# Optimization experiments

Measured on AMD Instinct MI355X. Metric: run time of the kernel, lower is better.

## Reference

```python
import jax, jax.numpy as jnp
import numpy as np

N, D, O, H, T, S, R, BN = 4096, 256, 256, 256, 512, 8, 4, 2  # nodes, in, out, hidden, text_len, adj_size, relations used, basis_num


def setup_inputs() -> dict:
    key = jax.random.key(0)
    ks = jax.random.split(key, 16)
    sc = 0.05
    return {
        "entity_embeddings": jax.random.normal(ks[0], (N, D), jnp.float32) * sc,
        "text_encodings": jax.random.normal(ks[1], (1, T, 2 * H), jnp.float32) * sc,
        "adj_to_use": jnp.arange(R, dtype=jnp.int32),
        "adj_masks": jax.random.randint(ks[2], (R, N, N), 0, 2, dtype=jnp.int32),
        "text_guids": jax.random.normal(ks[3], (S, 2 * H), jnp.float32) * sc,
        "graph_guids_1": jax.random.normal(ks[4], (S, D), jnp.float32) * sc,
        "graph_guids_2": jax.random.normal(ks[5], (S, D), jnp.float32) * sc,
        "guid_a": jax.random.normal(ks[6], (S,), jnp.float32),
        "basis_V": jax.random.normal(ks[7], (D, BN, O), jnp.float32) * sc,
        "basis_b": jax.random.normal(ks[8], (S, BN), jnp.float32) * sc,
        "W_1": jax.random.normal(ks[9], (2 * H, D), jnp.float32) * sc,
        "W_2": jax.random.normal(ks[10], (2 * H, D), jnp.float32) * sc,
        "ln_gamma": jnp.ones((O,), jnp.float32),
        "ln_beta": jnp.zeros((O,), jnp.float32),
    }


def reference(entity_embeddings, text_encodings, adj_to_use, adj_masks,
              text_guids, graph_guids_1, graph_guids_2, guid_a,
              basis_V, basis_b, W_1, W_2, ln_gamma, ln_beta):
    te = text_encodings[0]                                  # [T, 2H] (batch of 1)
    tg = text_guids[adj_to_use]                             # [R, 2H]
    # text attention: softmax over T, per relation
    att = jax.nn.softmax(te @ tg.T, axis=0)                 # [T, R]
    context = att.T @ te                                    # [R, 2H]
    c1 = context @ W_1                                      # [R, D]
    c2 = context @ W_2
    ga = jax.nn.sigmoid(guid_a[adj_to_use])[:, None]        # [R, 1]
    g1 = ga * graph_guids_1[adj_to_use] + (1.0 - ga) * c1   # [R, D]
    g2 = ga * graph_guids_2[adj_to_use] + (1.0 - ga) * c2
    s1 = entity_embeddings @ g1.T                           # [N, R]
    s2 = entity_embeddings @ g2.T
    # A[r,i,j] = s1[i,r] + s2[j,r], masked softmax over j
    A = s1.T[:, :, None] + s2.T[:, None, :]                 # [R, N, N]
    A = jnp.where(adj_masks == 1, A, jnp.float32(-1e10))
    A = jax.nn.softmax(A, axis=-1)
    fused = jnp.einsum('rij,jd->rid', A, entity_embeddings) # [R, N, D]
    # torch.cat over relations on last dim -> column index r*D + d
    fused_cat = jnp.transpose(fused, (1, 0, 2)).reshape(N, R * D)
    # torch.matmul([R,BN],[D,BN,O]) -> [D,R,O], then .view(R*D, O) (row index d*R + r)
    bb = basis_b[adj_to_use]                                # [R, BN]
    W = jnp.einsum('rb,dbo->dro', bb, basis_V).reshape(D * R, O)
    out = fused_cat @ W                                     # [N, O]
    mu = jnp.mean(out, axis=-1, keepdims=True)
    var = jnp.var(out, axis=-1, keepdims=True)
    out = (out - mu) / jnp.sqrt(var + 1e-5) * ln_gamma + ln_beta
    return jax.nn.relu(out)
```

## Files before the change

kernel.cpp:

```cpp
#include <hip/hip_runtime.h>
#include <hip/hip_bf16.h>


typedef unsigned short u16;
typedef short bf16x8 __attribute__((ext_vector_type(8)));
typedef float f32x4 __attribute__((ext_vector_type(4)));
typedef float f32x8 __attribute__((ext_vector_type(8)));
typedef int   v4i   __attribute__((ext_vector_type(4)));
typedef unsigned int v2u __attribute__((ext_vector_type(2)));

#define G2_OFF    0
#define SC_OFF    4096
#define CTX_OFF   16384
#define WRT_OFF   69632
#define FPT_OFF   593920
#define FUSED_OFF 9506816
#define CAN_OFF   26284032

__device__ __forceinline__ float b2f(u16 u) {
    union { unsigned int i; float f; } v; v.i = ((unsigned int)u) << 16; return v.f;
}
__device__ __forceinline__ u16 f2b(float f) {
    union { float f; unsigned int i; } v; v.f = f;
    return (u16)((v.i + 0x7FFFu + ((v.i >> 16) & 1u)) >> 16);
}
__device__ __forceinline__ float rawf(const void* p, bool isbf, int i) {
    return isbf ? b2f(((const u16*)p)[i]) : ((const float*)p)[i];
}
__device__ __forceinline__ f32x8 raw8(const void* p, bool isbf, int i8) {
    f32x8 o;
    if (isbf) {
        bf16x8 v = *(const bf16x8*)((const u16*)p + i8);
        #pragma unroll
        for (int k = 0; k < 8; ++k) o[k] = b2f((u16)v[k]);
    } else {
        const float* f = (const float*)p + i8;
        float4 a = *(const float4*)f, b = *(const float4*)(f + 4);
        o[0] = a.x; o[1] = a.y; o[2] = a.z; o[3] = a.w;
        o[4] = b.x; o[5] = b.y; o[6] = b.z; o[7] = b.w;
    }
    return o;
}

__global__ __launch_bounds__(512) void k_front(
    const void* __restrict__ ent_raw, const void* __restrict__ te_raw,
    const int* __restrict__ adj, const void* __restrict__ tg_raw,
    const void* __restrict__ bV_raw, const void* __restrict__ bb_raw,
    const unsigned* __restrict__ graw,
    u16* __restrict__ ent_can, float* __restrict__ sc_ws, u16* __restrict__ wrt)
{
    bool isbf = (graw[0] == 0x3F803F80u);
    int b = blockIdx.x, tid = threadIdx.x;
    if (b < 256) {
        int base = b * 4096 + tid;
        if (isbf) {
            const u16* s = (const u16*)ent_raw;
            #pragma unroll
            for (int k = 0; k < 8; ++k) { int i = base + k * 512; ent_can[i] = s[i]; }
        } else {
            const float* s = (const float*)ent_raw;
            #pragma unroll
            for (int k = 0; k < 8; ++k) { int i = base + k * 512; ent_can[i] = f2b(s[i]); }
        }
        return;
    }
    if (b < 384) {
        int b2 = b - 256;
        int r = b2 >> 5, cq = b2 & 31;
        int c = cq * 8 + (tid >> 6);
        int dq = tid & 63;
        int a[4] = {adj[0], adj[1], adj[2], adj[3]};
        #pragma unroll
        for (int dd = 0; dd < 4; ++dd) {
            float w = 0.f;
            #pragma unroll
            for (int bi = 0; bi < 2; ++bi)
                w += rawf(bb_raw, isbf, a[dd] * 2 + bi) *
                     rawf(bV_raw, isbf, ((64 * r + dq) * 2 + bi) * 256 + c);
            wrt[(r * 256 + c) * 256 + dq * 4 + dd] = f2b(w);
        }
        return;
    }
    __shared__ float s_tg[4 * 512];
    int a[4] = {adj[0], adj[1], adj[2], adj[3]};
    for (int idx = tid; idx < 2048; idx += 512) {
        int r = idx >> 9, h = idx & 511;
        s_tg[r * 512 + h] = rawf(tg_raw, isbf, a[r] * 512 + h);
    }
    __syncthreads();
    int b2 = b - 384;
    int t = b2 * 16 + (tid >> 5);
    int h0 = (tid & 31) * 16;
    float s[4] = {0.f, 0.f, 0.f, 0.f};
    #pragma unroll
    for (int half = 0; half < 2; ++half) {
        f32x8 v = raw8(te_raw, isbf, t * 512 + h0 + half * 8);
        #pragma unroll
        for (int k = 0; k < 8; ++k) {
            float tv = v[k]; int h = h0 + half * 8 + k;
            #pragma unroll
            for (int r = 0; r < 4; ++r) s[r] += tv * s_tg[r * 512 + h];
        }
    }
    #pragma unroll
    for (int r = 0; r < 4; ++r) {
        #pragma unroll
        for (int m = 16; m > 0; m >>= 1) s[r] += __shfl_xor(s[r], m);
    }
    if ((tid & 31) == 0) {
        #pragma unroll
        for (int r = 0; r < 4; ++r) sc_ws[t * 4 + r] = s[r];
    }
}

__global__ __launch_bounds__(256) void k_ctx(const void* __restrict__ te_raw,
                                             const float* __restrict__ sc_ws,
                                             const unsigned* __restrict__ graw,
                                             float* __restrict__ ctx_ws) {
    bool isbf = (graw[0] == 0x3F803F80u);
    __shared__ float s_att[512];
    __shared__ float s_red[256];
    __shared__ float s_part[32 * 8];
    int b = blockIdx.x, tid = threadIdx.x;
    int r = b >> 6, hc = b & 63;
    float v0 = sc_ws[tid * 4 + r], v1 = sc_ws[(tid + 256) * 4 + r];
    s_red[tid] = fmaxf(v0, v1);
    __syncthreads();
    for (int st = 128; st > 0; st >>= 1) {
        if (tid < st) s_red[tid] = fmaxf(s_red[tid], s_red[tid + st]);
        __syncthreads();
    }
    float mx = s_red[0];
    __syncthreads();
    float e0 = __expf(v0 - mx), e1 = __expf(v1 - mx);
    s_red[tid] = e0 + e1;
    __syncthreads();
    for (int st = 128; st > 0; st >>= 1) {
        if (tid < st) s_red[tid] += s_red[tid + st];
        __syncthreads();
    }
    float rdn = 1.f / s_red[0];
    __syncthreads();
    s_att[tid] = e0 * rdn;
    s_att[tid + 256] = e1 * rdn;
    __syncthreads();
    int hl = tid & 7, tq = tid >> 3;
    int h = hc * 8 + hl;
    float acc = 0.f;
    #pragma unroll 4
    for (int t = tq * 16; t < tq * 16 + 16; ++t)
        acc += s_att[t] * rawf(te_raw, isbf, t * 512 + h);
    s_part[tq * 8 + hl] = acc;
    __syncthreads();
    if (tid < 8) {
        float c = 0.f;
        #pragma unroll
        for (int s = 0; s < 32; ++s) c += s_part[s * 8 + tid];
        ctx_ws[r * 512 + hc * 8 + tid] = c;
    }
}

__global__ __launch_bounds__(256) void k_g2(const float* __restrict__ ctx_ws,
                                            const int* __restrict__ adj,
                                            const void* __restrict__ W2_raw,
                                            const void* __restrict__ gg2_raw,
                                            const void* __restrict__ ga_raw,
                                            const unsigned* __restrict__ graw,
                                            float* __restrict__ g2ws) {
    bool isbf = (graw[0] == 0x3F803F80u);
    __shared__ float s_ctx[512];
    __shared__ float s_p[2][128];
    int b = blockIdx.x, tid = threadIdx.x;
    int r = b >> 1, dh = b & 1;
    for (int idx = tid; idx < 512; idx += 256) s_ctx[idx] = ctx_ws[r * 512 + idx];
    __syncthreads();
    int dl = tid & 127, th = tid >> 7;
    int d = dh * 128 + dl;
    float acc = 0.f;
    for (int h = th * 256; h < th * 256 + 256; ++h)
        acc += s_ctx[h] * rawf(W2_raw, isbf, h * 256 + d);
    s_p[th][dl] = acc;
    __syncthreads();
    if (th == 0) {
        float tot = s_p[0][dl] + s_p[1][dl];
        int ar = adj[r];
        float gav = 1.f / (1.f + expf(-rawf(ga_raw, isbf, ar)));
        g2ws[r * 256 + d] = gav * rawf(gg2_raw, isbf, ar * 256 + d) + (1.f - gav) * tot;
    }
}

__global__ __launch_bounds__(512) void k_fplus(const u16* __restrict__ entity,
                                               const u16* __restrict__ wrt,
                                               const float* __restrict__ g2ws,
                                               u16* __restrict__ fpt) {
    int b = blockIdx.x, tid = threadIdx.x;
    int r = b & 3, ct = (b >> 2) & 3, jt = b >> 4;
    int c0 = ct * 64, j0 = jt * 256;
    __shared__ __align__(16) u16 lw[64 * 264];
    __shared__ float sg2[256];
    __shared__ float sE[256];
    const u16* wr = wrt + (r * 256 + c0) * 256;
    #pragma unroll
    for (int k = 0; k < 4; ++k) {
        int ci = tid + k * 512; int row = ci >> 5, off = (ci & 31) * 8;
        *(v4i*)(&lw[row * 264 + off]) = *(const v4i*)(wr + row * 256 + off);
    }
    if (tid < 256) sg2[tid] = g2ws[r * 256 + tid];
    __syncthreads();
    int wv = tid >> 6, lane = tid & 63, ln = lane & 15, q = lane >> 4;
    {
        float gl0 = sg2[lane * 4 + 0], gl1 = sg2[lane * 4 + 1];
        float gl2 = sg2[lane * 4 + 2], gl3 = sg2[lane * 4 + 3];
        #pragma unroll 4
        for (int i = 0; i < 32; ++i) {
            int row = j0 + wv * 32 + i;
            v2u e4 = *(const v2u*)(entity + row * 256 + lane * 4);
            float s = b2f((u16)(e4.x & 0xFFFFu)) * gl0
                    + b2f((u16)(e4.x >> 16))     * gl1
                    + b2f((u16)(e4.y & 0xFFFFu)) * gl2
                    + b2f((u16)(e4.y >> 16))     * gl3;
            #pragma unroll
            for (int m = 32; m > 0; m >>= 1) s += __shfl_xor(s, m);
            if (lane == 0) sE[wv * 32 + i] = expf(s);
        }
    }
    __syncthreads();
    f32x4 acc[4][2] = {};
    for (int ks = 0; ks < 8; ++ks) {
        bf16x8 afr[4], bfr[2];
        #pragma unroll
        for (int mt = 0; mt < 4; ++mt)
            afr[mt] = *(const bf16x8*)(&lw[(mt * 16 + ln) * 264 + ks * 32 + q * 8]);
        #pragma unroll
        for (int nt = 0; nt < 2; ++nt) {
            int j = j0 + (wv * 2 + nt) * 16 + ln;
            bfr[nt] = *(const bf16x8*)(entity + j * 256 + ks * 32 + q * 8);
        }
        #pragma unroll
        for (int mt = 0; mt < 4; ++mt)
            #pragma unroll
            for (int nt = 0; nt < 2; ++nt)
                acc[mt][nt] = __builtin_amdgcn_mfma_f32_16x16x32_bf16(afr[mt], bfr[nt], acc[mt][nt], 0, 0, 0);
    }
    #pragma unroll
    for (int nt = 0; nt < 2; ++nt) {
        int jl = (wv * 2 + nt) * 16 + ln;
        int j = j0 + jl;
        float e2j = sE[jl];
        int kt = j >> 5, kk = j & 31;
        u16* dst = fpt + (((size_t)(r * 128 + kt)) * 272 << 5);
        #pragma unroll
        for (int mt = 0; mt < 4; ++mt)
            #pragma unroll
            for (int reg = 0; reg < 4; ++reg) {
                int c = c0 + mt * 16 + q * 4 + reg;
                dst[(c << 5) + kk] = f2b(acc[mt][nt][reg] * e2j);
            }
    }
    if (ct == 0) {
        #pragma unroll
        for (int s = 0; s < 8; ++s) {
            int l = s * 512 + tid;
            int kk = l & 31, cl = (l >> 5) & 15, ktl = l >> 9;
            int kt = jt * 8 + ktl;
            fpt[(((size_t)(r * 128 + kt) * 272 + 256 + cl) << 5) + kk] =
                (cl == 0) ? f2b(sE[ktl * 32 + kk]) : (u16)0;
        }
    }
}

__global__ __launch_bounds__(512) void k_big(const int* __restrict__ masks,
                                             const u16* __restrict__ fpt,
                                             float* __restrict__ fused) {
    __shared__ __align__(16) u16 lm[2][64 * 32];
    __shared__ __align__(16) u16 lf[2][272 * 32];
    __shared__ float lden[64];
    int b = blockIdx.x, tid = threadIdx.x;
    int xcd = b & 7; int r = xcd & 3;
    int it = (b >> 3) + ((xcd >> 2) << 5);
    long i0 = (long)it * 64;
    const int* mbase = masks + ((long)r << 24) + i0 * 4096;
    const u16* fbase = fpt + (size_t)r * 128 * 272 * 32;
    int wave = tid >> 6, lane = tid & 63, ln = lane & 15, q = lane >> 4;
    int mg = wave >> 2, ng = wave & 3;
    int swb = (ln >> 1) & 3;
    int rq = (q ^ swb) * 8;
    int srow = tid >> 2, sch = tid & 3;
    int ssw = (sch ^ ((srow >> 1) & 3)) * 8;

    f32x4 acc[2][4] = {};
    f32x4 accD0 = {}, accD1 = {};

    struct Slot { v4i pm0, pm1, f0, f1, f2; };
    Slot s0, s1, s2, s3;
    auto load_slot = [&](int kt, Slot& s) {
        const u16* su = fbase + (size_t)kt * 8704;
        s.f0 = *(const v4i*)(su + tid * 8);
        s.f1 = *(const v4i*)(su + (tid + 512) * 8);
        if (tid < 64) s.f2 = *(const v4i*)(su + (tid + 1024) * 8);
        if (tid < 256) {
            const int* mp = mbase + srow * 4096 + kt * 32 + sch * 8;
            s.pm0 = __builtin_nontemporal_load((const v4i*)mp);
            s.pm1 = __builtin_nontemporal_load((const v4i*)(mp + 4));
        }
    };
    auto stage = [&](int par, const Slot& s) {
        u16* dst = &lf[par][0];
        *(v4i*)(dst + srow * 32 + ssw) = s.f0;
        *(v4i*)(dst + (128 + srow) * 32 + ssw) = s.f1;
        if (tid < 64) *(v4i*)(dst + (256 + srow) * 32 + ssw) = s.f2;
        if (tid < 256) {
            unsigned m0 = (unsigned)s.pm0.x * 0x3F80u, m1 = (unsigned)s.pm0.y * 0x3F80u;
            unsigned m2 = (unsigned)s.pm0.z * 0x3F80u, m3 = (unsigned)s.pm0.w * 0x3F80u;
            unsigned m4 = (unsigned)s.pm1.x * 0x3F80u, m5 = (unsigned)s.pm1.y * 0x3F80u;
            unsigned m6 = (unsigned)s.pm1.z * 0x3F80u, m7 = (unsigned)s.pm1.w * 0x3F80u;
            v4i w;
            w.x = (int)(m0 | (m1 << 16)); w.y = (int)(m2 | (m3 << 16));
            w.z = (int)(m4 | (m5 << 16)); w.w = (int)(m6 | (m7 << 16));
            *(v4i*)(&lm[par][srow * 32 + ssw]) = w;
        }
    };
    auto step = [&](int k, Slot& sM, Slot& sF) {
        const u16* msrc = &lm[k & 1][0];
        const u16* src  = &lf[k & 1][0];
        bf16x8 a0 = *(const bf16x8*)(msrc + (mg * 32 + ln) * 32 + rq);
        bf16x8 a1 = *(const bf16x8*)(msrc + (mg * 32 + 16 + ln) * 32 + rq);
        if (k + 1 < 128) stage((k + 1) & 1, sF);
        if (k + 4 < 128) load_slot(k + 4, sM);
        #pragma unroll
        for (int nt = 0; nt < 4; ++nt) {
            bf16x8 bf = *(const bf16x8*)(src + ((ng * 4 + nt) * 16 + ln) * 32 + rq);
            acc[0][nt] = __builtin_amdgcn_mfma_f32_16x16x32_bf16(a0, bf, acc[0][nt], 0, 0, 0);
            acc[1][nt] = __builtin_amdgcn_mfma_f32_16x16x32_bf16(a1, bf, acc[1][nt], 0, 0, 0);
        }
        if (ng == 3) {
            bf16x8 bf = *(const bf16x8*)(src + (256 + ln) * 32 + rq);
            accD0 = __builtin_amdgcn_mfma_f32_16x16x32_bf16(a0, bf, accD0, 0, 0, 0);
            accD1 = __builtin_amdgcn_mfma_f32_16x16x32_bf16(a1, bf, accD1, 0, 0, 0);
        }
        __syncthreads();
    };

    load_slot(0, s0);
    load_slot(1, s1);
    load_slot(2, s2);
    load_slot(3, s3);
    stage(0, s0);
    __syncthreads();
    #pragma unroll 1
    for (int kt = 0; kt < 128; kt += 4) {
        step(kt,     s0, s1);
        step(kt + 1, s1, s2);
        step(kt + 2, s2, s3);
        step(kt + 3, s3, s0);
    }

    if (ng == 3 && ln == 0) {
        #pragma unroll
        for (int reg = 0; reg < 4; ++reg) {
            lden[mg * 32 + q * 4 + reg]      = accD0[reg];
            lden[mg * 32 + 16 + q * 4 + reg] = accD1[reg];
        }
    }
    __syncthreads();
    float* fb = fused + ((long)r * 4096 + i0) * 256;
    #pragma unroll
    for (int mt = 0; mt < 2; ++mt) {
        float rd[4];
        #pragma unroll
        for (int reg = 0; reg < 4; ++reg) rd[reg] = 1.0f / lden[mg * 32 + mt * 16 + q * 4 + reg];
        #pragma unroll
        for (int nt = 0; nt < 4; ++nt) {
            int c = (ng * 4 + nt) * 16 + ln;
            #pragma unroll
            for (int reg = 0; reg < 4; ++reg) {
                int row = mg * 32 + mt * 16 + q * 4 + reg;
                __builtin_nontemporal_store(acc[mt][nt][reg] * rd[reg], fb + row * 256 + c);
            }
        }
    }
}

__global__ __launch_bounds__(256) void k_ln(const float* __restrict__ fused,
                                            const void* __restrict__ gamma_raw,
                                            const void* __restrict__ beta_raw,
                                            const unsigned* __restrict__ graw,
                                            void* __restrict__ outraw) {
    __shared__ float part[8];
    int i = blockIdx.x, o = threadIdx.x;
    bool isbf = (graw[0] == 0x3F803F80u);
    float x = 0.f;
    for (int r = 0; r < 4; ++r)
        x += __builtin_nontemporal_load(fused + ((long)(r << 12) + i) * 256 + o);
    float s = x;
    #pragma unroll
    for (int st = 32; st > 0; st >>= 1) s += __shfl_xor(s, st);
    int w = o >> 6;
    if ((o & 63) == 0) part[w] = s;
    __syncthreads();
    float mu = (part[0] + part[1] + part[2] + part[3]) * (1.f / 256.f);
    float v = x - mu;
    float qv = v * v;
    #pragma unroll
    for (int st = 32; st > 0; st >>= 1) qv += __shfl_xor(qv, st);
    if ((o & 63) == 0) part[4 + w] = qv;
    __syncthreads();
    float var = (part[4] + part[5] + part[6] + part[7]) * (1.f / 256.f);
    float y = v * rsqrtf(var + 1e-5f) * rawf(gamma_raw, isbf, o) + rawf(beta_raw, isbf, o);
    float res = fmaxf(y, 0.f);
    if (isbf) ((u16*)outraw)[i * 256 + o] = f2b(res);
    else      ((float*)outraw)[i * 256 + o] = res;
}

extern "C" void kernel_launch(void* const* d_in, const int* in_sizes, int n_in,
                              void* d_out, int out_size, void* d_ws, size_t ws_size,
                              hipStream_t stream) {
    const int* adj   = (const int*)d_in[2];
    const int* masks = (const int*)d_in[3];
    const unsigned* graw = (const unsigned*)d_in[12];
    char* ws = (char*)d_ws;
    float* g2ws = (float*)(ws + G2_OFF);
    float* scws = (float*)(ws + SC_OFF);
    float* ctxw = (float*)(ws + CTX_OFF);
    u16*   wrt  = (u16*)(ws + WRT_OFF);
    u16*   fpt  = (u16*)(ws + FPT_OFF);
    float* fus  = (float*)(ws + FUSED_OFF);
    u16*   ent  = (u16*)(ws + CAN_OFF);

    k_front<<<416, 512, 0, stream>>>(d_in[0], d_in[1], adj, d_in[4],
                                     d_in[8], d_in[9], graw, ent, scws, wrt);
    k_ctx<<<256, 256, 0, stream>>>(d_in[1], scws, graw, ctxw);
    k_g2<<<8, 256, 0, stream>>>(ctxw, adj, d_in[11], d_in[6], d_in[7], graw, g2ws);
    k_fplus<<<256, 512, 0, stream>>>(ent, wrt, g2ws, fpt);
    k_big<<<256, 512, 0, stream>>>(masks, fpt, fus);
    k_ln<<<4096, 256, 0, stream>>>(fus, d_in[12], d_in[13], graw, d_out);
}
```

Before: 494.2 us.

## Bit-pack adjacency masks in a front pre-pass and expand bits in k_big

Adds 1024 blocks to k_front that stream the int32 adjacency masks and pack them into 32-bit ballot words laid out per relation, k-tile and row. k_big then loads one word per row per k-tile instead of 32 int32 mask values, and expands bits into bf16 MFMA A-fragments in registers. This drops the LDS mask staging buffer and most of the mask global loads from the MFMA main loop. The full mask read still happens, now in the separate pre-pass, which also does strided 4-byte stores from a single lane and uses an extra 8 MB of workspace.

Measured after the change: 615.5 us. 24.5% more time.

```diff
diff --git a/kernel.cpp b/kernel.cpp
--- a/kernel.cpp
+++ b/kernel.cpp
@@ -16,6 +16,7 @@
 #define FPT_OFF   593920
 #define FUSED_OFF 9506816
 #define CAN_OFF   26284032
+#define PMK_OFF   28381184
 
 __device__ __forceinline__ float b2f(u16 u) {
     union { unsigned int i; float f; } v; v.i = ((unsigned int)u) << 16; return v.f;
@@ -46,8 +47,9 @@
     const void* __restrict__ ent_raw, const void* __restrict__ te_raw,
     const int* __restrict__ adj, const void* __restrict__ tg_raw,
     const void* __restrict__ bV_raw, const void* __restrict__ bb_raw,
-    const unsigned* __restrict__ graw,
-    u16* __restrict__ ent_can, float* __restrict__ sc_ws, u16* __restrict__ wrt)
+    const unsigned* __restrict__ graw, const int* __restrict__ masks,
+    u16* __restrict__ ent_can, float* __restrict__ sc_ws,
+    u16* __restrict__ wrt, unsigned* __restrict__ pmk)
 {
     bool isbf = (graw[0] == 0x3F803F80u);
     int b = blockIdx.x, tid = threadIdx.x;
@@ -81,35 +83,56 @@
         }
         return;
     }
-    __shared__ float s_tg[4 * 512];
-    int a[4] = {adj[0], adj[1], adj[2], adj[3]};
-    for (int idx = tid; idx < 2048; idx += 512) {
-        int r = idx >> 9, h = idx & 511;
-        s_tg[r * 512 + h] = rawf(tg_raw, isbf, a[r] * 512 + h);
-    }
-    __syncthreads();
-    int b2 = b - 384;
-    int t = b2 * 16 + (tid >> 5);
-    int h0 = (tid & 31) * 16;
-    float s[4] = {0.f, 0.f, 0.f, 0.f};
-    #pragma unroll
-    for (int half = 0; half < 2; ++half) {
-        f32x8 v = raw8(te_raw, isbf, t * 512 + h0 + half * 8);
-        #pragma unroll
-        for (int k = 0; k < 8; ++k) {
-            float tv = v[k]; int h = h0 + half * 8 + k;
-            #pragma unroll
-            for (int r = 0; r < 4; ++r) s[r] += tv * s_tg[r * 512 + h];
-        }
-    }
-    #pragma unroll
-    for (int r = 0; r < 4; ++r) {
-        #pragma unroll
-        for (int m = 16; m > 0; m >>= 1) s[r] += __shfl_xor(s[r], m);
-    }
-    if ((tid & 31) == 0) {
-        #pragma unroll
-        for (int r = 0; r < 4; ++r) sc_ws[t * 4 + r] = s[r];
+    if (b < 416) {
+        __shared__ float s_tg[4 * 512];
+        int a[4] = {adj[0], adj[1], adj[2], adj[3]};
+        for (int idx = tid; idx < 2048; idx += 512) {
+            int r = idx >> 9, h = idx & 511;
+            s_tg[r * 512 + h] = rawf(tg_raw, isbf, a[r] * 512 + h);
+        }
+        __syncthreads();
+        int b2 = b - 384;
+        int t = b2 * 16 + (tid >> 5);
+        int h0 = (tid & 31) * 16;
+        float s[4] = {0.f, 0.f, 0.f, 0.f};
+        #pragma unroll
+        for (int half = 0; half < 2; ++half) {
+            f32x8 v = raw8(te_raw, isbf, t * 512 + h0 + half * 8);
+            #pragma unroll
+            for (int k = 0; k < 8; ++k) {
+                float tv = v[k]; int h = h0 + half * 8 + k;
+                #pragma unroll
+                for (int r = 0; r < 4; ++r) s[r] += tv * s_tg[r * 512 + h];
+            }
+        }
+        #pragma unroll
+        for (int r = 0; r < 4; ++r) {
+            #pragma unroll
+            for (int m = 16; m > 0; m >>= 1) s[r] += __shfl_xor(s[r], m);
+        }
+        if ((tid & 31) == 0) {
+            #pragma unroll
+            for (int r = 0; r < 4; ++r) sc_ws[t * 4 + r] = s[r];
+        }
+        return;
+    }
+    int pb = b - 416;
+    int wv = tid >> 6, lane = tid & 63;
+    #pragma unroll
+    for (int rr = 0; rr < 2; ++rr) {
+        int rid = pb * 16 + wv * 2 + rr;
+        int r = rid >> 12, i = rid & 4095;
+        const int* mp = masks + ((((long)r << 12) + i) << 12) + lane;
+        unsigned* dst = pmk + ((size_t)r * 128) * 4096 + i;
+        #pragma unroll 4
+        for (int c = 0; c < 64; ++c) {
+            int m = mp[c * 64];
+            unsigned long long bits = __ballot(m != 0);
+            if (lane == 0) {
+                dst[(size_t)(c * 2) * 4096]     = (unsigned)bits;
+                dst[(size_t)(c * 2 + 1) * 4096] = (unsigned)(bits >> 32);
+            }
+        }
     }
 }
 
@@ -269,62 +292,63 @@
     }
 }
 
-__global__ __launch_bounds__(512) void k_big(const int* __restrict__ masks,
+__global__ __launch_bounds__(512) void k_big(const unsigned* __restrict__ pmk,
                                              const u16* __restrict__ fpt,
                                              float* __restrict__ fused) {
-    __shared__ __align__(16) u16 lm[2][64 * 32];
     __shared__ __align__(16) u16 lf[2][272 * 32];
+    __shared__ unsigned ldsw[2][64];
     __shared__ float lden[64];
     int b = blockIdx.x, tid = threadIdx.x;
     int xcd = b & 7; int r = xcd & 3;
     int it = (b >> 3) + ((xcd >> 2) << 5);
     long i0 = (long)it * 64;
-    const int* mbase = masks + ((long)r << 24) + i0 * 4096;
+    const unsigned* pbase = pmk + (size_t)r * 128 * 4096 + i0;
     const u16* fbase = fpt + (size_t)r * 128 * 272 * 32;
     int wave = tid >> 6, lane = tid & 63, ln = lane & 15, q = lane >> 4;
     int mg = wave >> 2, ng = wave & 3;
     int swb = (ln >> 1) & 3;
     int rq = (q ^ swb) * 8;
-    int srow = tid >> 2, sch = tid & 3;
-    int ssw = (sch ^ ((srow >> 1) & 3)) * 8;
+    int srowF = tid >> 2, schF = tid & 3;
+    int sswF = (schF ^ ((srowF >> 1) & 3)) * 8;
 
     f32x4 acc[2][4] = {};
     f32x4 accD0 = {}, accD1 = {};
 
-    struct Slot { v4i pm0, pm1, f0, f1, f2; };
+    auto expand = [](unsigned byte) -> bf16x8 {
+        v4i w;
+        w.x = (int)(((byte & 1u) * 0x3F80u)        | (((byte >> 1) & 1u) * 0x3F800000u));
+        w.y = (int)((((byte >> 2) & 1u) * 0x3F80u) | (((byte >> 3) & 1u) * 0x3F800000u));
+        w.z = (int)((((byte >> 4) & 1u) * 0x3F80u) | (((byte >> 5) & 1u) * 0x3F800000u));
+        w.w = (int)((((byte >> 6) & 1u) * 0x3F80u) | (((byte >> 7) & 1u) * 0x3F800000u));
+        union { v4i i; bf16x8 h; } u; u.i = w; return u.h;
+    };
+
+    struct Slot { v4i f0, f1, f2; unsigned w; };
     Slot s0, s1, s2, s3;
     auto load_slot = [&](int kt, Slot& s) {
         const u16* su = fbase + (size_t)kt * 8704;
         s.f0 = *(const v4i*)(su + tid * 8);
         s.f1 = *(const v4i*)(su + (tid + 512) * 8);
-        if (tid < 64) s.f2 = *(const v4i*)(su + (tid + 1024) * 8);
-        if (tid < 256) {
-            const int* mp = mbase + srow * 4096 + kt * 32 + sch * 8;
-            s.pm0 = __builtin_nontemporal_load((const v4i*)mp);
-            s.pm1 = __builtin_nontemporal_load((const v4i*)(mp + 4));
+        if (tid < 64) {
+            s.f2 = *(const v4i*)(su + (tid + 1024) * 8);
+            s.w  = pbase[(size_t)kt * 4096 + tid];
         }
     };
     auto stage = [&](int par, const Slot& s) {
         u16* dst = &lf[par][0];
-        *(v4i*)(dst + srow * 32 + ssw) = s.f0;
-        *(v4i*)(dst + (128 + srow) * 32 + ssw) = s.f1;
-        if (tid < 64) *(v4i*)(dst + (256 + srow) * 32 + ssw) = s.f2;
-        if (tid < 256) {
-            unsigned m0 = (unsigned)s.pm0.x * 0x3F80u, m1 = (unsigned)s.pm0.y * 0x3F80u;
-            unsigned m2 = (unsigned)s.pm0.z * 0x3F80u, m3 = (unsigned)s.pm0.w * 0x3F80u;
-            unsigned m4 = (unsigned)s.pm1.x * 0x3F80u, m5 = (unsigned)s.pm1.y * 0x3F80u;
-            unsigned m6 = (unsigned)s.pm1.z * 0x3F80u, m7 = (unsigned)s.pm1.w * 0x3F80u;
-            v4i w;
-            w.x = (int)(m0 | (m1 << 16)); w.y = (int)(m2 | (m3 << 16));
-            w.z = (int)(m4 | (m5 << 16)); w.w = (int)(m6 | (m7 << 16));
-            *(v4i*)(&lm[par][srow * 32 + ssw]) = w;
+        *(v4i*)(dst + srowF * 32 + sswF) = s.f0;
+        *(v4i*)(dst + (128 + srowF) * 32 + sswF) = s.f1;
+        if (tid < 64) {
+            *(v4i*)(dst + (256 + srowF) * 32 + sswF) = s.f2;
+            ldsw[par][tid] = s.w;
         }
     };
     auto step = [&](int k, Slot& sM, Slot& sF) {
-        const u16* msrc = &lm[k & 1][0];
-        const u16* src  = &lf[k & 1][0];
-        bf16x8 a0 = *(const bf16x8*)(msrc + (mg * 32 + ln) * 32 + rq);
-        bf16x8 a1 = *(const bf16x8*)(msrc + (mg * 32 + 16 + ln) * 32 + rq);
+        const u16* src = &lf[k & 1][0];
+        unsigned w0 = ldsw[k & 1][mg * 32 + ln];
+        unsigned w1 = ldsw[k & 1][mg * 32 + 16 + ln];
+        bf16x8 a0 = expand((w0 >> (q * 8)) & 0xFFu);
+        bf16x8 a1 = expand((w1 >> (q * 8)) & 0xFFu);
         if (k + 1 < 128) stage((k + 1) & 1, sF);
         if (k + 4 < 128) load_slot(k + 4, sM);
         #pragma unroll
@@ -426,12 +450,14 @@
     u16*   fpt  = (u16*)(ws + FPT_OFF);
     float* fus  = (float*)(ws + FUSED_OFF);
     u16*   ent  = (u16*)(ws + CAN_OFF);
-
-    k_front<<<416, 512, 0, stream>>>(d_in[0], d_in[1], adj, d_in[4],
-                                     d_in[8], d_in[9], graw, ent, scws, wrt);
+    unsigned* pmk = (unsigned*)(ws + PMK_OFF);
+
+    k_front<<<1440, 512, 0, stream>>>(d_in[0], d_in[1], adj, d_in[4],
+                                      d_in[8], d_in[9], graw, masks,
+                                      ent, scws, wrt, pmk);
     k_ctx<<<256, 256, 0, stream>>>(d_in[1], scws, graw, ctxw);
     k_g2<<<8, 256, 0, stream>>>(ctxw, adj, d_in[11], d_in[6], d_in[7], graw, g2ws);
     k_fplus<<<256, 512, 0, stream>>>(ent, wrt, g2ws, fpt);
-    k_big<<<256, 512, 0, stream>>>(masks, fpt, fus);
+    k_big<<<256, 512, 0, stream>>>(pmk, fpt, fus);
     k_ln<<<4096, 256, 0, stream>>>(fus, d_in[12], d_in[13], graw, d_out);
 }
```
